# Kernel tuning notes

Hardware: AMD Instinct MI355X
Metric: run time of the kernel (lower is better)

Reference implementation:

```python
import jax, jax.numpy as jnp
import numpy as np

B, N, D = 8, 2048, 512
H, DH = 8, 64
SCALE = DH ** -0.5


def setup_inputs() -> dict:
    key = jax.random.key(0)
    ks = jax.random.split(key, 7)
    x = jax.random.normal(ks[0], (B, N, D), dtype=jnp.float32)
    mask = jax.random.uniform(ks[1], (B, N, N), dtype=jnp.float32)
    Wq = jax.random.normal(ks[2], (D, H * DH), dtype=jnp.float32) * (D ** -0.5)
    Wk = jax.random.normal(ks[3], (D, H * DH), dtype=jnp.float32) * (D ** -0.5)
    Wv = jax.random.normal(ks[4], (D, H * DH), dtype=jnp.float32) * (D ** -0.5)
    Wo = jax.random.normal(ks[5], (H * DH, D), dtype=jnp.float32) * ((H * DH) ** -0.5)
    bo = jnp.zeros((D,), dtype=jnp.float32)
    return {"x": x, "mask": mask, "Wq": Wq, "Wk": Wk, "Wv": Wv, "Wo": Wo, "bo": bo}


def reference(x, mask, Wq, Wk, Wv, Wo, bo):
    b, n, d = x.shape
    # QKV projections -> [b, h, n, dh]
    q = (x @ Wq).reshape(b, n, H, DH).transpose(0, 2, 1, 3)
    k = (x @ Wk).reshape(b, n, H, DH).transpose(0, 2, 1, 3)
    v = (x @ Wv).reshape(b, n, H, DH).transpose(0, 2, 1, 3)
    # scores with multiplicative structural mask bias: dots * (1 + M)
    dots = jnp.einsum('bhid,bhjd->bhij', q, k) * SCALE
    dots = dots * (1.0 + mask[:, None, :, :])
    attn = jax.nn.softmax(dots, axis=-1)  # dropout is identity in eval
    out = jnp.einsum('bhij,bhjd->bhid', attn, v)
    out = out.transpose(0, 2, 1, 3).reshape(b, n, H * DH)
    return out @ Wo + bo
```

## Files before the change

### kernel.cpp

```cpp
#include <hip/hip_runtime.h>

typedef __bf16 bf16;
typedef __bf16 bf16x8 __attribute__((ext_vector_type(8)));
typedef float  f32x4  __attribute__((ext_vector_type(4)));
typedef unsigned u32x4 __attribute__((ext_vector_type(4)));

#define B_  8
#define N_  2048
#define D_  512
#define H_  8
#define DH_ 64
static constexpr float SC2 = 0.18033688011112042f;

#if defined(__has_builtin)
#if __has_builtin(__builtin_amdgcn_exp2f)
#define EXP2(x) __builtin_amdgcn_exp2f(x)
#else
#define EXP2(x) exp2f(x)
#endif
#else
#define EXP2(x) exp2f(x)
#endif

#if defined(__has_builtin)
#if __has_builtin(__builtin_amdgcn_permlane32_swap) && __has_builtin(__builtin_amdgcn_permlane16_swap)
#define HAVE_PLSWAP 1
#endif
#endif

__device__ __forceinline__ f32x4 mfma16(bf16x8 a, bf16x8 b, f32x4 c) {
  return __builtin_amdgcn_mfma_f32_16x16x32_bf16(a, b, c, 0, 0, 0);
}

__device__ __forceinline__ void gload_lds16(const void* g, void* l) {
  __builtin_amdgcn_global_load_lds((__attribute__((address_space(1))) void*)g,
                                   (__attribute__((address_space(3))) void*)l, 16, 0, 0);
}

__device__ __forceinline__ unsigned cvt_pk_bf16(float lo, float hi) {
  unsigned r;
  asm("v_cvt_pk_bf16_f32 %0, %1, %2" : "=v"(r) : "v"(lo), "v"(hi));
  return r;
}

__global__ void k_cvt_x(const float* __restrict__ x, bf16* __restrict__ xb) {
  int i = blockIdx.x * blockDim.x + threadIdx.x;
  const float4* p = (const float4*)x;
  float4 a = p[2*i], b = p[2*i+1];
  bf16x8 o;
  o[0]=(bf16)a.x; o[1]=(bf16)a.y; o[2]=(bf16)a.z; o[3]=(bf16)a.w;
  o[4]=(bf16)b.x; o[5]=(bf16)b.y; o[6]=(bf16)b.z; o[7]=(bf16)b.w;
  ((bf16x8*)xb)[i] = o;
}

__global__ void k_wt(const float* __restrict__ w, bf16* __restrict__ wt) {
  __shared__ float t[64][65];
  const int c0 = blockIdx.x * 64, k0 = blockIdx.y * 64;
  const int r = threadIdx.x >> 2, q4 = (threadIdx.x & 3) * 16;
#pragma unroll
  for (int j = 0; j < 16; j += 4) {
    float4 v = *(const float4*)(w + (k0 + r) * 512 + c0 + q4 + j);
    t[r][q4+j] = v.x; t[r][q4+j+1] = v.y; t[r][q4+j+2] = v.z; t[r][q4+j+3] = v.w;
  }
  __syncthreads();
  const int c = threadIdx.x >> 2, kq = (threadIdx.x & 3) * 16;
  bf16x8 o0, o1;
#pragma unroll
  for (int j = 0; j < 8; ++j) { o0[j] = (bf16)t[kq+j][c]; o1[j] = (bf16)t[kq+8+j][c]; }
  *(bf16x8*)(wt + (c0 + c) * 512 + k0 + kq) = o0;
  *(bf16x8*)(wt + (c0 + c) * 512 + k0 + kq + 8) = o1;
}

template<int MODE>
__global__ void k_gemm(const bf16* __restrict__ A, const bf16* __restrict__ Bt,
                       bf16* __restrict__ qo, bf16* __restrict__ ko, bf16* __restrict__ vo,
                       float* __restrict__ outp, const float* __restrict__ bo) {
  __shared__ bf16 lA[128 * 64];
  __shared__ bf16 lB[128 * 64];
  const int tid = threadIdx.x;
  const int wid = tid >> 6, lane = tid & 63;
  const int l15 = lane & 15, lq = lane >> 4;
  const int wr = wid >> 1, wc = wid & 1;
  const long long rowtile = (long long)blockIdx.x * 128;
  const long long coltile = (long long)blockIdx.y * 128;

  const bf16* gA[4]; const bf16* gB[4];
  bf16* lAc[4]; bf16* lBc[4];
#pragma unroll
  for (int i = 0; i < 4; ++i) {
    int ci = wid * 4 + i;
    int row = ci * 8 + (lane >> 3);
    int c8 = (lane & 7) ^ (row & 7);
    gA[i] = A + (rowtile + row) * 512 + c8 * 8;
    gB[i] = Bt + (coltile + row) * 512 + c8 * 8;
    lAc[i] = &lA[ci * 512];
    lBc[i] = &lB[ci * 512];
  }
  unsigned aoff[4][2], boff[4][2];
#pragma unroll
  for (int mi = 0; mi < 4; ++mi) {
#pragma unroll
    for (int ks = 0; ks < 2; ++ks) {
      int R = l15 + 16 * mi + 64 * wr;
      aoff[mi][ks] = R * 128 + ((((ks << 2) | lq) ^ (R & 7)) << 4);
      int Rb = l15 + 16 * mi + 64 * wc;
      boff[mi][ks] = Rb * 128 + ((((ks << 2) | lq) ^ (Rb & 7)) << 4);
    }
  }
  f32x4 acc[4][4] = {};
  for (int kt = 0; kt < 8; ++kt) {
#pragma unroll
    for (int i = 0; i < 4; ++i) gload_lds16(gA[i], lAc[i]);
#pragma unroll
    for (int i = 0; i < 4; ++i) gload_lds16(gB[i], lBc[i]);
#pragma unroll
    for (int i = 0; i < 4; ++i) { gA[i] += 64; gB[i] += 64; }
    __syncthreads();
#pragma unroll
    for (int ks = 0; ks < 2; ++ks) {
      bf16x8 af[4], bfr[4];
#pragma unroll
      for (int mi = 0; mi < 4; ++mi) af[mi] = *(const bf16x8*)((const char*)lA + aoff[mi][ks]);
#pragma unroll
      for (int nf = 0; nf < 4; ++nf) bfr[nf] = *(const bf16x8*)((const char*)lB + boff[nf][ks]);
#pragma unroll
      for (int mi = 0; mi < 4; ++mi)
#pragma unroll
        for (int nf = 0; nf < 4; ++nf)
          acc[mi][nf] = mfma16(af[mi], bfr[nf], acc[mi][nf]);
    }
    __syncthreads();
  }
  if (MODE == 0) {
#pragma unroll
    for (int nf = 0; nf < 4; ++nf) {
      const int col = (int)coltile + 64 * wc + nf * 16 + l15;
      const int mat = col >> 9, c5 = col & 511, hh = c5 >> 6, dh = c5 & 63;
#pragma unroll
      for (int mi = 0; mi < 4; ++mi) {
#pragma unroll
        for (int r = 0; r < 4; ++r) {
          const int R = (int)rowtile + 64 * wr + mi * 16 + lq * 4 + r;
          const int bb = R >> 11, n = R & 2047;
          const bf16 bv = (bf16)acc[mi][nf][r];
          const long long bh = bb * 8 + hh;
          if (mat == 0)      qo[(bh * 2048 + n) * 64 + dh] = bv;
          else if (mat == 1) ko[(bh * 2048 + n) * 64 + dh] = bv;
          else               vo[(bh * 64 + dh) * 2048 + n] = bv;
        }
      }
    }
  } else {
#pragma unroll
    for (int nf = 0; nf < 4; ++nf) {
      const int col = (int)coltile + 64 * wc + nf * 16 + l15;
      const float bias = bo[col];
#pragma unroll
      for (int mi = 0; mi < 4; ++mi)
#pragma unroll
        for (int r = 0; r < 4; ++r) {
          const long long R = rowtile + 64 * wr + mi * 16 + lq * 4 + r;
          outp[R * 512 + col] = acc[mi][nf][r] + bias;
        }
    }
  }
}

__global__ __attribute__((amdgpu_flat_work_group_size(512, 512),
                          amdgpu_waves_per_eu(4))) void k_attn(
    const bf16* __restrict__ qb, const bf16* __restrict__ kb, const bf16* __restrict__ vt,
    const float* __restrict__ mask, bf16* __restrict__ ao) {
  __shared__ __align__(16) bf16 kvls[2][2][64 * 64];
  const int tid = threadIdx.x;
  const int wid = tid >> 6, lane = tid & 63;
  const int l15 = lane & 15, lq = lane >> 4;
  const int p = blockIdx.x;
  const int xcd = p & 7, kk = p >> 3;
  const int g = xcd * 16 + (kk >> 3), h = kk & 7;
  const int b = g >> 4, qt = g & 15;
  const long long bh = b * 8 + h;
  const bf16* Q = qb + bh * (2048ll * 64);
  const bf16* K = kb + bh * (2048ll * 64);
  const bf16* V = vt + bh * (64ll * 2048);
  const int qrow0 = qt * 128 + wid * 16;
  const float* mptr = mask + ((long long)b * 2048 + qrow0 + l15) * 2048 + lq * 4;

  const int srow = tid >> 3;
  const int sc = (tid & 7) ^ (srow & 7);
  const bf16* kg = K + srow * 64 + sc * 8;
  const bf16* vg = V + srow * 2048 + sc * 8;

  bf16x8 qf[2];
#pragma unroll
  for (int ks = 0; ks < 2; ++ks)
    qf[ks] = *(const bf16x8*)(Q + (qrow0 + l15) * 64 + ks * 32 + lq * 8);

  f32x4 o[4] = {};
  float lsum = 0.f;
  f32x4 mA[4], mB[4];

  auto stageKV = [&](int buf, int jt) {
    gload_lds16(kg + jt * 4096, &kvls[buf][0][tid * 8]);
    gload_lds16(vg + jt * 64,   &kvls[buf][1][tid * 8]);
  };
  auto mload = [&](f32x4 (&m)[4], int jb) {
#pragma unroll
    for (int nf = 0; nf < 4; ++nf)
      m[nf] = *(const f32x4*)(mptr + jb + nf * 16);
  };

  auto compute = [&](int buf, const f32x4 (&m)[4]) {
    const bf16* kbL = &kvls[buf][0][0];
    const bf16* vbL = &kvls[buf][1][0];
    f32x4 s[4];
#pragma unroll
    for (int nf = 0; nf < 4; ++nf) {
      const int row = nf * 16 + l15;
      const bf16x8 kf = *(const bf16x8*)(kbL + row * 64 + ((lq ^ (row & 7)) << 3));
      f32x4 z = {0.f, 0.f, 0.f, 0.f};
      s[nf] = mfma16(kf, qf[0], z);
    }
#pragma unroll
    for (int nf = 0; nf < 4; ++nf) {
      const int row = nf * 16 + l15;
      const bf16x8 kf = *(const bf16x8*)(kbL + row * 64 + (((4 + lq) ^ (row & 7)) << 3));
      s[nf] = mfma16(kf, qf[1], s[nf]);
    }
    unsigned w[4][2];
#pragma unroll
    for (int nf = 0; nf < 4; ++nf) {
      float mp0 = fmaf(m[nf][0], SC2, SC2);
      float mp1 = fmaf(m[nf][1], SC2, SC2);
      float mp2 = fmaf(m[nf][2], SC2, SC2);
      float mp3 = fmaf(m[nf][3], SC2, SC2);
      float pe0 = EXP2(s[nf][0] * mp0);
      float pe1 = EXP2(s[nf][1] * mp1);
      float pe2 = EXP2(s[nf][2] * mp2);
      float pe3 = EXP2(s[nf][3] * mp3);
      lsum += ((pe0 + pe1) + (pe2 + pe3));
      w[nf][0] = cvt_pk_bf16(pe0, pe1);
      w[nf][1] = cvt_pk_bf16(pe2, pe3);
    }
    unsigned pa0[4], pa1[4];
#ifdef HAVE_PLSWAP
#pragma unroll
    for (int t = 0; t < 2; ++t) {
      auto sA = __builtin_amdgcn_permlane32_swap(w[0][t], w[1][t], false, false);
      auto sB = __builtin_amdgcn_permlane16_swap(sA[0], sA[1], false, false);
      pa0[t] = sB[0]; pa0[t + 2] = sB[1];
      auto sC = __builtin_amdgcn_permlane32_swap(w[2][t], w[3][t], false, false);
      auto sD = __builtin_amdgcn_permlane16_swap(sC[0], sC[1], false, false);
      pa1[t] = sD[0]; pa1[t + 2] = sD[1];
    }
#else
    {
      const int basel = l15 + ((lq & 1) << 5);
#pragma unroll
      for (int t = 0; t < 2; ++t) {
        int sel0 = (lq & 2) ? (int)w[1][t] : (int)w[0][t];
        int sel1 = (lq & 2) ? (int)w[3][t] : (int)w[2][t];
        pa0[t]     = (unsigned)__shfl(sel0, basel);
        pa0[t + 2] = (unsigned)__shfl(sel0, basel + 16);
        pa1[t]     = (unsigned)__shfl(sel1, basel);
        pa1[t + 2] = (unsigned)__shfl(sel1, basel + 16);
      }
    }
#endif
    u32x4 ua = {pa0[0], pa0[1], pa0[2], pa0[3]};
    u32x4 ub = {pa1[0], pa1[1], pa1[2], pa1[3]};
    const bf16x8 paA = __builtin_bit_cast(bf16x8, ua);
    const bf16x8 paB = __builtin_bit_cast(bf16x8, ub);
#pragma unroll
    for (int nf = 0; nf < 4; ++nf) {
      const int row = nf * 16 + l15;
      const bf16x8 vf = *(const bf16x8*)(vbL + row * 64 + ((lq ^ (row & 7)) << 3));
      o[nf] = mfma16(paA, vf, o[nf]);
    }
#pragma unroll
    for (int nf = 0; nf < 4; ++nf) {
      const int row = nf * 16 + l15;
      const bf16x8 vf = *(const bf16x8*)(vbL + row * 64 + (((4 + lq) ^ (row & 7)) << 3));
      o[nf] = mfma16(paB, vf, o[nf]);
    }
  };

  stageKV(0, 0);
  mload(mA, 0);
  __syncthreads();

  for (int jt = 0; jt < 32; jt += 2) {
    stageKV(1, jt + 1);
    mload(mB, (jt + 1) * 64);
    compute(0, mA);
    __syncthreads();
    if (jt + 2 < 32) {
      stageKV(0, jt + 2);
      mload(mA, (jt + 2) * 64);
    }
    compute(1, mB);
    __syncthreads();
  }

  lsum += __shfl_xor(lsum, 16);
  lsum += __shfl_xor(lsum, 32);
  const float rinv = 1.0f / lsum;
  float rv[4];
#pragma unroll
  for (int r = 0; r < 4; ++r)
    rv[r] = __shfl(rinv, ((lane & 48) >> 2) + r);
#pragma unroll
  for (int nf = 0; nf < 4; ++nf)
#pragma unroll
    for (int r = 0; r < 4; ++r) {
      const long long rowg = (long long)b * 2048 + qrow0 + lq * 4 + r;
      ao[rowg * 512 + h * 64 + nf * 16 + l15] = (bf16)(o[nf][r] * rv[r]);
    }
}

extern "C" void kernel_launch(void* const* d_in, const int* in_sizes, int n_in,
                              void* d_out, int out_size, void* d_ws, size_t ws_size,
                              hipStream_t stream) {
  const float* x    = (const float*)d_in[0];
  const float* mask = (const float*)d_in[1];
  const float* Wq   = (const float*)d_in[2];
  const float* Wk   = (const float*)d_in[3];
  const float* Wv   = (const float*)d_in[4];
  const float* Wo   = (const float*)d_in[5];
  const float* bo   = (const float*)d_in[6];
  float* out = (float*)d_out;
  char* ws = (char*)d_ws;

  const size_t SZ_XB = (size_t)16384 * 512 * 2;
  const size_t SZ_W3 = (size_t)1536 * 512 * 2;
  const size_t SZ_WO = (size_t)512 * 512 * 2;
  const size_t SZ_T  = (size_t)64 * 2048 * 64 * 2;

  bf16* xb    = (bf16*)ws;
  bf16* wqkvT = (bf16*)(ws + SZ_XB);
  bf16* woT   = (bf16*)(ws + SZ_XB + SZ_W3);
  bf16* qbuf  = (bf16*)(ws + SZ_XB + SZ_W3 + SZ_WO);
  bf16* kbuf  = (bf16*)((char*)qbuf + SZ_T);
  bf16* vtb   = (bf16*)((char*)kbuf + SZ_T);
  bf16* aob   = xb;

  k_cvt_x<<<dim3(4096), dim3(256), 0, stream>>>(x, xb);
  k_wt<<<dim3(8, 8), dim3(256), 0, stream>>>(Wq, wqkvT);
  k_wt<<<dim3(8, 8), dim3(256), 0, stream>>>(Wk, wqkvT + 512 * 512);
  k_wt<<<dim3(8, 8), dim3(256), 0, stream>>>(Wv, wqkvT + 2 * 512 * 512);
  k_wt<<<dim3(8, 8), dim3(256), 0, stream>>>(Wo, woT);
  k_gemm<0><<<dim3(128, 12), dim3(256), 0, stream>>>(xb, wqkvT, qbuf, kbuf, vtb, nullptr, nullptr);
  k_attn<<<dim3(1024), dim3(512), 0, stream>>>(qbuf, kbuf, vtb, mask, aob);
  k_gemm<1><<<dim3(128, 4), dim3(256), 0, stream>>>(aob, woT, nullptr, nullptr, nullptr, out, bo);
}
```

Baseline: 249.6 us.

## Give each attention wave two query tiles to reuse K/V fragments

The attention kernel now runs 256-thread blocks of 4 waves, and each wave handles 32 query rows (two 16-row tiles) instead of 16. Each K and V LDS fragment read therefore feeds two MFMAs, which halves LDS read traffic per FLOP, and each thread stages twice as much K/V per tile. The loop is restructured to single-buffer steps with the mask prefetch moved into the softmax helper. In exchange, register pressure rises with doubled accumulators and mask buffers, and occupancy bounds change.

```diff
diff --git a/kernel.cpp b/kernel.cpp
--- a/kernel.cpp
+++ b/kernel.cpp
@@ -166,13 +166,13 @@
   }
 }
 
-__global__ __attribute__((amdgpu_flat_work_group_size(512, 512),
-                          amdgpu_waves_per_eu(4))) void k_attn(
+__global__ __launch_bounds__(256, 3) void k_attn(
     const bf16* __restrict__ qb, const bf16* __restrict__ kb, const bf16* __restrict__ vt,
     const float* __restrict__ mask, bf16* __restrict__ ao) {
   __shared__ __align__(16) bf16 kvls[2][2][64 * 64];
   const int tid = threadIdx.x;
-  const int wid = tid >> 6, lane = tid & 63;
+  const int lane = tid & 63;
+  const int wid = tid >> 6;
   const int l15 = lane & 15, lq = lane >> 4;
   const int p = blockIdx.x;
   const int xcd = p & 7, kk = p >> 3;
@@ -182,50 +182,36 @@
   const bf16* Q = qb + bh * (2048ll * 64);
   const bf16* K = kb + bh * (2048ll * 64);
   const bf16* V = vt + bh * (64ll * 2048);
-  const int qrow0 = qt * 128 + wid * 16;
-  const float* mptr = mask + ((long long)b * 2048 + qrow0 + l15) * 2048 + lq * 4;
-
-  const int srow = tid >> 3;
-  const int sc = (tid & 7) ^ (srow & 7);
-  const bf16* kg = K + srow * 64 + sc * 8;
-  const bf16* vg = V + srow * 2048 + sc * 8;
-
-  bf16x8 qf[2];
-#pragma unroll
-  for (int ks = 0; ks < 2; ++ks)
-    qf[ks] = *(const bf16x8*)(Q + (qrow0 + l15) * 64 + ks * 32 + lq * 8);
-
-  f32x4 o[4] = {};
-  float lsum = 0.f;
+  const int qrow0 = qt * 128 + wid * 32;
+  const float* mptr0 = mask + ((long long)b * 2048 + qrow0 + l15) * 2048 + lq * 4;
+  const float* mptr1 = mptr0 + 16 * 2048;
+
+  const int row0 = tid >> 3, row1 = row0 + 32;
+  const int sc = (tid & 7) ^ (row0 & 7);
+  const bf16* kg0 = K + row0 * 64 + sc * 8;
+  const bf16* vg0 = V + row0 * 2048 + sc * 8;
+  const bf16* vg1 = V + row1 * 2048 + sc * 8;
+
+  bf16x8 qf[2][2];
+#pragma unroll
+  for (int mi = 0; mi < 2; ++mi)
+#pragma unroll
+    for (int ks = 0; ks < 2; ++ks)
+      qf[mi][ks] = *(const bf16x8*)(Q + (qrow0 + mi * 16 + l15) * 64 + ks * 32 + lq * 8);
+
+  f32x4 o[2][4] = {};
+  float lsum0 = 0.f, lsum1 = 0.f;
   f32x4 mA[4], mB[4];
 
   auto stageKV = [&](int buf, int jt) {
-    gload_lds16(kg + jt * 4096, &kvls[buf][0][tid * 8]);
-    gload_lds16(vg + jt * 64,   &kvls[buf][1][tid * 8]);
+    gload_lds16(kg0 + jt * 4096,        &kvls[buf][0][tid * 8]);
+    gload_lds16(kg0 + jt * 4096 + 2048, &kvls[buf][0][tid * 8 + 2048]);
+    gload_lds16(vg0 + jt * 64,          &kvls[buf][1][tid * 8]);
+    gload_lds16(vg1 + jt * 64,          &kvls[buf][1][tid * 8 + 2048]);
   };
-  auto mload = [&](f32x4 (&m)[4], int jb) {
-#pragma unroll
-    for (int nf = 0; nf < 4; ++nf)
-      m[nf] = *(const f32x4*)(mptr + jb + nf * 16);
-  };
-
-  auto compute = [&](int buf, const f32x4 (&m)[4]) {
-    const bf16* kbL = &kvls[buf][0][0];
-    const bf16* vbL = &kvls[buf][1][0];
-    f32x4 s[4];
-#pragma unroll
-    for (int nf = 0; nf < 4; ++nf) {
-      const int row = nf * 16 + l15;
-      const bf16x8 kf = *(const bf16x8*)(kbL + row * 64 + ((lq ^ (row & 7)) << 3));
-      f32x4 z = {0.f, 0.f, 0.f, 0.f};
-      s[nf] = mfma16(kf, qf[0], z);
-    }
-#pragma unroll
-    for (int nf = 0; nf < 4; ++nf) {
-      const int row = nf * 16 + l15;
-      const bf16x8 kf = *(const bf16x8*)(kbL + row * 64 + (((4 + lq) ^ (row & 7)) << 3));
-      s[nf] = mfma16(kf, qf[1], s[nf]);
-    }
+
+  auto smax = [&](f32x4 (&m)[4], const float* mp, const f32x4 (&sm)[4], float& ls,
+                  bf16x8& pA, bf16x8& pB, bool pref, int jbn) {
     unsigned w[4][2];
 #pragma unroll
     for (int nf = 0; nf < 4; ++nf) {
@@ -233,13 +219,18 @@
       float mp1 = fmaf(m[nf][1], SC2, SC2);
       float mp2 = fmaf(m[nf][2], SC2, SC2);
       float mp3 = fmaf(m[nf][3], SC2, SC2);
-      float pe0 = EXP2(s[nf][0] * mp0);
-      float pe1 = EXP2(s[nf][1] * mp1);
-      float pe2 = EXP2(s[nf][2] * mp2);
-      float pe3 = EXP2(s[nf][3] * mp3);
-      lsum += ((pe0 + pe1) + (pe2 + pe3));
+      float pe0 = EXP2(sm[nf][0] * mp0);
+      float pe1 = EXP2(sm[nf][1] * mp1);
+      float pe2 = EXP2(sm[nf][2] * mp2);
+      float pe3 = EXP2(sm[nf][3] * mp3);
+      ls += ((pe0 + pe1) + (pe2 + pe3));
       w[nf][0] = cvt_pk_bf16(pe0, pe1);
       w[nf][1] = cvt_pk_bf16(pe2, pe3);
+    }
+    if (pref) {
+#pragma unroll
+      for (int nf = 0; nf < 4; ++nf)
+        m[nf] = *(const f32x4*)(mp + jbn + nf * 16);
     }
     unsigned pa0[4], pa1[4];
 #ifdef HAVE_PLSWAP
@@ -268,53 +259,88 @@
 #endif
     u32x4 ua = {pa0[0], pa0[1], pa0[2], pa0[3]};
     u32x4 ub = {pa1[0], pa1[1], pa1[2], pa1[3]};
-    const bf16x8 paA = __builtin_bit_cast(bf16x8, ua);
-    const bf16x8 paB = __builtin_bit_cast(bf16x8, ub);
+    pA = __builtin_bit_cast(bf16x8, ua);
+    pB = __builtin_bit_cast(bf16x8, ub);
+  };
+
+  stageKV(0, 0);
+#pragma unroll
+  for (int nf = 0; nf < 4; ++nf) {
+    mA[nf] = *(const f32x4*)(mptr0 + nf * 16);
+    mB[nf] = *(const f32x4*)(mptr1 + nf * 16);
+  }
+  __syncthreads();
+
+  for (int jt = 0; jt < 32; ++jt) {
+    const int buf = jt & 1;
+    const bool morejt = (jt + 1 < 32);
+    if (morejt) stageKV(buf ^ 1, jt + 1);
+    const bf16* kbL = &kvls[buf][0][0];
+    const bf16* vbL = &kvls[buf][1][0];
+
+    f32x4 s[2][4];
+    {
+      bf16x8 kf0[4], kf1[4];
+#pragma unroll
+      for (int nf = 0; nf < 4; ++nf) {
+        const int row = nf * 16 + l15;
+        kf0[nf] = *(const bf16x8*)(kbL + row * 64 + ((lq ^ (row & 7)) << 3));
+        kf1[nf] = *(const bf16x8*)(kbL + row * 64 + (((4 + lq) ^ (row & 7)) << 3));
+      }
+#pragma unroll
+      for (int mi = 0; mi < 2; ++mi)
+#pragma unroll
+        for (int nf = 0; nf < 4; ++nf) {
+          f32x4 z = {0.f, 0.f, 0.f, 0.f};
+          s[mi][nf] = mfma16(kf0[nf], qf[mi][0], z);
+        }
+#pragma unroll
+      for (int mi = 0; mi < 2; ++mi)
+#pragma unroll
+        for (int nf = 0; nf < 4; ++nf)
+          s[mi][nf] = mfma16(kf1[nf], qf[mi][1], s[mi][nf]);
+    }
+
+    bf16x8 paA0, paB0, paA1, paB1;
+    smax(mA, mptr0, s[0], lsum0, paA0, paB0, morejt, (jt + 1) * 64);
+    smax(mB, mptr1, s[1], lsum1, paA1, paB1, morejt, (jt + 1) * 64);
+
 #pragma unroll
     for (int nf = 0; nf < 4; ++nf) {
       const int row = nf * 16 + l15;
       const bf16x8 vf = *(const bf16x8*)(vbL + row * 64 + ((lq ^ (row & 7)) << 3));
-      o[nf] = mfma16(paA, vf, o[nf]);
+      o[0][nf] = mfma16(paA0, vf, o[0][nf]);
+      o[1][nf] = mfma16(paA1, vf, o[1][nf]);
     }
 #pragma unroll
     for (int nf = 0; nf < 4; ++nf) {
       const int row = nf * 16 + l15;
       const bf16x8 vf = *(const bf16x8*)(vbL + row * 64 + (((4 + lq) ^ (row & 7)) << 3));
-      o[nf] = mfma16(paB, vf, o[nf]);
-    }
-  };
-
-  stageKV(0, 0);
-  mload(mA, 0);
-  __syncthreads();
-
-  for (int jt = 0; jt < 32; jt += 2) {
-    stageKV(1, jt + 1);
-    mload(mB, (jt + 1) * 64);
-    compute(0, mA);
+      o[0][nf] = mfma16(paB0, vf, o[0][nf]);
+      o[1][nf] = mfma16(paB1, vf, o[1][nf]);
+    }
     __syncthreads();
-    if (jt + 2 < 32) {
-      stageKV(0, jt + 2);
-      mload(mA, (jt + 2) * 64);
-    }
-    compute(1, mB);
-    __syncthreads();
-  }
-
-  lsum += __shfl_xor(lsum, 16);
-  lsum += __shfl_xor(lsum, 32);
-  const float rinv = 1.0f / lsum;
-  float rv[4];
-#pragma unroll
-  for (int r = 0; r < 4; ++r)
-    rv[r] = __shfl(rinv, ((lane & 48) >> 2) + r);
-#pragma unroll
-  for (int nf = 0; nf < 4; ++nf)
-#pragma unroll
-    for (int r = 0; r < 4; ++r) {
-      const long long rowg = (long long)b * 2048 + qrow0 + lq * 4 + r;
-      ao[rowg * 512 + h * 64 + nf * 16 + l15] = (bf16)(o[nf][r] * rv[r]);
-    }
+  }
+
+  float v0 = lsum0, v1 = lsum1;
+  v0 += __shfl_xor(v0, 16); v0 += __shfl_xor(v0, 32);
+  v1 += __shfl_xor(v1, 16); v1 += __shfl_xor(v1, 32);
+  const float ri0 = 1.0f / v0, ri1 = 1.0f / v1;
+  float rv[2][4];
+#pragma unroll
+  for (int r = 0; r < 4; ++r) {
+    rv[0][r] = __shfl(ri0, ((lane & 48) >> 2) + r);
+    rv[1][r] = __shfl(ri1, ((lane & 48) >> 2) + r);
+  }
+#pragma unroll
+  for (int mi = 0; mi < 2; ++mi)
+#pragma unroll
+    for (int nf = 0; nf < 4; ++nf)
+#pragma unroll
+      for (int r = 0; r < 4; ++r) {
+        const long long rowg = (long long)b * 2048 + qrow0 + mi * 16 + lq * 4 + r;
+        ao[rowg * 512 + h * 64 + nf * 16 + l15] = (bf16)(o[mi][nf][r] * rv[mi][r]);
+      }
 }
 
 extern "C" void kernel_launch(void* const* d_in, const int* in_sizes, int n_in,
@@ -349,6 +375,6 @@
   k_wt<<<dim3(8, 8), dim3(256), 0, stream>>>(Wv, wqkvT + 2 * 512 * 512);
   k_wt<<<dim3(8, 8), dim3(256), 0, stream>>>(Wo, woT);
   k_gemm<0><<<dim3(128, 12), dim3(256), 0, stream>>>(xb, wqkvT, qbuf, kbuf, vtb, nullptr, nullptr);
-  k_attn<<<dim3(1024), dim3(512), 0, stream>>>(qbuf, kbuf, vtb, mask, aob);
+  k_attn<<<dim3(1024), dim3(256), 0, stream>>>(qbuf, kbuf, vtb, mask, aob);
   k_gemm<1><<<dim3(128, 4), dim3(256), 0, stream>>>(aob, woT, nullptr, nullptr, nullptr, out, bo);
 }
```

Result: slower. 256.1 us (+2.6%).
